# Optimization experiments

Measured on AMD Instinct MI355X. Metric: run time of the kernel, lower is better.

The kernel has to match this reference:

```python
import jax, jax.numpy as jnp
import numpy as np

DIM = 512
NUM_HEADS = 8
HEAD_DIM = DIM // NUM_HEADS


def setup_inputs() -> dict:
    key = jax.random.key(0)
    ks = jax.random.split(key, 9)
    s = 1.0 / np.sqrt(DIM)
    x = jax.random.normal(ks[0], (2, 4096, DIM), dtype=jnp.float32)
    Wq = jax.random.uniform(ks[1], (DIM, DIM), jnp.float32, -s, s)
    bq = jax.random.uniform(ks[2], (DIM,), jnp.float32, -s, s)
    Wk = jax.random.uniform(ks[3], (DIM, DIM), jnp.float32, -s, s)
    bk = jax.random.uniform(ks[4], (DIM,), jnp.float32, -s, s)
    Wv = jax.random.uniform(ks[5], (DIM, DIM), jnp.float32, -s, s)
    bv = jax.random.uniform(ks[6], (DIM,), jnp.float32, -s, s)
    Wo = jax.random.uniform(ks[7], (DIM, DIM), jnp.float32, -s, s)
    bo = jax.random.uniform(ks[8], (DIM,), jnp.float32, -s, s)
    return {"x": x, "Wq": Wq, "bq": bq, "Wk": Wk, "bk": bk,
            "Wv": Wv, "bv": bv, "Wo": Wo, "bo": bo}


def reference(x, Wq, bq, Wk, bk, Wv, bv, Wo, bo):
    B, S, D = x.shape
    H, Hd = NUM_HEADS, HEAD_DIM
    # Linear layers (torch stores weight as [out,in]; here W is [in,out])
    q = (x @ Wq + bq).reshape(B, S, H, Hd).transpose(0, 2, 1, 3)  # [B,H,S,Hd]
    k = (x @ Wk + bk).reshape(B, S, H, Hd).transpose(0, 2, 1, 3)
    v = (x @ Wv + bv).reshape(B, S, H, Hd).transpose(0, 2, 1, 3)
    # NOTE: original scales by dim**0.5, not head_dim**0.5
    energy = jnp.einsum('bhqd,bhkd->bhqk', q, k) / jnp.sqrt(jnp.float32(D))
    attn = jax.nn.softmax(energy, axis=-1)
    out = jnp.einsum('bhqk,bhkd->bhqd', attn, v)
    out = out.transpose(0, 2, 1, 3).reshape(B, S, D)
    return out @ Wo + bo
```

## Files before the change

kernel.cpp:

```cpp
#include <hip/hip_runtime.h>

typedef unsigned short USH;
typedef short s16x8 __attribute__((ext_vector_type(8)));
typedef float f32x4 __attribute__((ext_vector_type(4)));
typedef float f32x4v __attribute__((ext_vector_type(4)));
typedef unsigned int u32x4 __attribute__((ext_vector_type(4)));
typedef s16x8 s16x8_a __attribute__((may_alias));
typedef f32x4v f32x4v_a __attribute__((may_alias));
typedef u32x4 u32x4_a __attribute__((may_alias));
typedef unsigned long long u64_a __attribute__((may_alias));

#if __has_builtin(__builtin_amdgcn_exp2f)
#define EXP2F(x) __builtin_amdgcn_exp2f(x)
#else
#define EXP2F(x) __builtin_exp2f(x)
#endif

__device__ __forceinline__ USH f2bf(float f) {
  union { float f; unsigned int i; } c; c.f = f;
  unsigned int x = c.i;
  return (USH)((x + 0x7FFFu + ((x >> 16) & 1u)) >> 16);
}
__device__ __forceinline__ unsigned int pk_bf16(float a, float b) {
#if __has_builtin(__builtin_amdgcn_cvt_pk_bf16_f32)
  typedef USH ush2 __attribute__((ext_vector_type(2)));
  union { ush2 v; unsigned int u; } r;
  r.v = __builtin_amdgcn_cvt_pk_bf16_f32(a, b);
  return r.u;
#else
  union { float f; unsigned int i; } ca, cb; ca.f = a; cb.f = b;
  return ((ca.i + 0x8000u) >> 16) | ((cb.i + 0x8000u) & 0xFFFF0000u);
#endif
}

__device__ __forceinline__ f32x4 mfma16(s16x8 a, s16x8 b, f32x4 c) {
  return __builtin_amdgcn_mfma_f32_16x16x32_bf16(a, b, c, 0, 0, 0);
}

#if __has_builtin(__builtin_amdgcn_global_load_lds)
__device__ __forceinline__ void gld_lds16(const void* g, void* l) {
  __builtin_amdgcn_global_load_lds(
      static_cast<const unsigned int __attribute__((address_space(1)))*>(
          (const void __attribute__((address_space(1)))*)g),
      static_cast<unsigned int __attribute__((address_space(3)))*>(
          (void __attribute__((address_space(3)))*)l),
      16, 0, 0);
}
#else
__device__ __forceinline__ void gld_lds16(const void* g, void* l) {
  *(s16x8_a*)l = *(const s16x8_a*)g;
}
#endif

__global__ __launch_bounds__(256) void prep(
    const float* __restrict__ Wq, const float* __restrict__ Wk,
    const float* __restrict__ Wv, const float* __restrict__ Wo,
    USH* __restrict__ wsT) {
  __shared__ float tile[32][33];
  const int z = blockIdx.z;
  const int t = threadIdx.x;
  const float* W = (z == 0) ? Wq : (z == 1) ? Wk : (z == 2) ? Wv : Wo;
  USH* WT = wsT + (size_t)z * 262144;
  const int n0 = blockIdx.x * 32, k0 = blockIdx.y * 32;
  const int tx = t & 31, ty = t >> 5;
  #pragma unroll
  for (int i = 0; i < 4; ++i)
    tile[ty + i * 8][tx] = W[(size_t)(k0 + ty + i * 8) * 512 + n0 + tx];
  __syncthreads();
  #pragma unroll
  for (int i = 0; i < 4; ++i)
    WT[(size_t)(n0 + ty + i * 8) * 512 + k0 + tx] = f2bf(tile[tx][ty + i * 8]);
}

template <int MODE>
__global__ __launch_bounds__(256, 3) void gemm_bias(
    const USH* __restrict__ A, const float* __restrict__ A32,
    const USH* __restrict__ BT0,
    const float* __restrict__ b0, const float* __restrict__ b1,
    const float* __restrict__ b2,
    USH* __restrict__ oQ, USH* __restrict__ oKV, float* __restrict__ oF) {
  __shared__ __align__(16) USH As[MODE == 1 ? 16384 : 8192];
  __shared__ __align__(16) USH Bs[8192];
  const int z = blockIdx.z;
  const USH* BT = BT0 + (size_t)z * 262144;
  const float* bias = (z == 0) ? b0 : ((z == 1) ? b1 : b2);
  USH* outb = (z == 0) ? oQ : (oKV + (size_t)(z - 1) * 4194304);
  const float qs = (MODE == 1 && z == 0) ? 0.06375871528132839f : 1.0f;

  const int t = threadIdx.x;
  const int w = t >> 6, lane = t & 63;
  const int c = lane & 15, g = lane >> 4;
  const int wm = w & 1, wn = w >> 1;
  const int m0 = blockIdx.x * 128, n0 = blockIdx.y * 128;

  f32x4 acc[4][4] = {};

  const int rB = w * 32 + (lane >> 3);
  const int ccB = (((lane & 7) ^ ((lane >> 3) & 7))) * 8;
  const USH* BpD = BT + (size_t)(n0 + rB) * 512 + ccB;
  USH* lB = Bs + w * 2048 + lane * 8;

  const USH* ApD = nullptr;
  USH* lA0 = nullptr;
  const float* Ap32 = nullptr;
  USH* lA1 = nullptr;
  if (MODE == 0) {
    ApD = A + (size_t)(m0 + rB) * 512 + ccB;
    lA0 = As + w * 2048 + lane * 8;
  } else {
    const int rA = w * 4 + (lane >> 4);
    const int gcA = (lane & 15) ^ (rA & 15);
    Ap32 = A32 + (size_t)(m0 + rA) * 512 + gcA * 4;
    lA1 = As + w * 512 + lane * 8;
  }

  for (int kt = 0; kt < 8; ++kt) {
    __syncthreads();
    if (MODE == 0) {
      #pragma unroll
      for (int j = 0; j < 4; ++j) {
        gld_lds16(ApD + kt * 64 + j * 4096, lA0 + j * 512);
        gld_lds16(BpD + kt * 64 + j * 4096, lB + j * 512);
      }
    } else {
      #pragma unroll
      for (int j = 0; j < 8; ++j)
        gld_lds16(Ap32 + kt * 64 + (size_t)j * 8192, lA1 + j * 2048);
      #pragma unroll
      for (int j = 0; j < 4; ++j)
        gld_lds16(BpD + kt * 64 + j * 4096, lB + j * 512);
    }
    __syncthreads();
    #pragma unroll
    for (int ks = 0; ks < 2; ++ks) {
      s16x8 af[4], bfr[4];
      #pragma unroll
      for (int i = 0; i < 4; ++i) {
        const int ra = wm * 64 + i * 16 + c;
        const int rb = wn * 64 + i * 16 + c;
        if (MODE == 0) {
          af[i] = *(const s16x8_a*)(As + ra * 64 + ((ks * 4 + g) ^ (ra & 7)) * 8);
        } else {
          const int e = ks * 4 + g;
          const int p0 = (2 * e) ^ (ra & 15), p1 = (2 * e + 1) ^ (ra & 15);
          const float* Af = (const float*)As + ra * 64;
          const f32x4v lo = *(const f32x4v_a*)(Af + p0 * 4);
          const f32x4v hi = *(const f32x4v_a*)(Af + p1 * 4);
          union { u32x4 u; s16x8 v; } cvt;
          cvt.u.x = pk_bf16(lo.x, lo.y); cvt.u.y = pk_bf16(lo.z, lo.w);
          cvt.u.z = pk_bf16(hi.x, hi.y); cvt.u.w = pk_bf16(hi.z, hi.w);
          af[i] = cvt.v;
        }
        bfr[i] = *(const s16x8_a*)(Bs + rb * 64 + ((ks * 4 + g) ^ (rb & 7)) * 8);
      }
      #pragma unroll
      for (int mf = 0; mf < 4; ++mf)
        #pragma unroll
        for (int nf = 0; nf < 4; ++nf)
          acc[mf][nf] = mfma16(af[mf], bfr[nf], acc[mf][nf]);
    }
  }

  #pragma unroll
  for (int nf = 0; nf < 4; ++nf) {
    const int n = n0 + wn * 64 + nf * 16 + c;
    const float bv = bias[n];
    #pragma unroll
    for (int mf = 0; mf < 4; ++mf)
      #pragma unroll
      for (int r = 0; r < 4; ++r) {
        const int m = m0 + wm * 64 + mf * 16 + g * 4 + r;
        const float v = (acc[mf][nf][r] + bv) * qs;
        if (MODE == 0) {
          oF[(size_t)m * 512 + n] = v;
        } else {
          const int bb = m >> 12, s = m & 4095, h = n >> 6, hd = n & 63;
          if (z == 2)
            outb[(((size_t)(bb * 8 + h)) * 64 + hd) * 4096 + s] = f2bf(v);
          else
            outb[(((size_t)(bb * 8 + h)) * 4096 + s) * 64 + hd] = f2bf(v);
        }
      }
  }
}

__global__ __launch_bounds__(512, 2) void attn(const USH* __restrict__ Qbuf,
                                               const USH* __restrict__ kv,
                                               USH* __restrict__ att) {
  __shared__ __align__(16) USH Ks[2 * 8192];
  __shared__ __align__(16) USH Vt[2 * 8192];
  __shared__ __align__(16) USH Ps[8][32 * 140];
  __shared__ float lbuf[8][32];

  const int t = threadIdx.x;
  const int w = t >> 6, lane = t & 63;
  const int c = lane & 15, g = lane >> 4;
  const int linear = blockIdx.x + (blockIdx.y << 4);
  const int xcd = linear & 7, idx = linear >> 3;
  const int bh = xcd + ((idx >> 4) << 3);
  const int bb = bh >> 3, hh = bh & 7;
  const size_t base = (size_t)bh * 262144;
  const USH* Q = Qbuf + base;
  const USH* K = kv + base;
  const USH* V = kv + 4194304 + base;
  const int q0 = (idx & 15) * 256 + w * 32;

  s16x8 qf[2][2];
  #pragma unroll
  for (int qi = 0; qi < 2; ++qi)
    #pragma unroll
    for (int kh = 0; kh < 2; ++kh)
      qf[qi][kh] = *(const s16x8_a*)(Q + (size_t)(q0 + qi * 16 + c) * 64 + kh * 32 + g * 8);

  s16x8 onesf;
  {
    const short one = (short)0x3F80, val = (c == 0) ? one : (short)0;
    #pragma unroll
    for (int j = 0; j < 8; ++j) onesf[j] = val;
  }

  f32x4 o[2][4] = {};
  f32x4 o_l[2] = {};

  const int keyK = w * 16 + (lane >> 2);
  const int ccK = (lane & 3) ^ ((keyK >> 1) & 3);
  const USH* gK0 = K + (size_t)keyK * 64 + ccK * 8;
  const int hdV = w * 4 + (lane >> 4);
  const int ccV = (lane & 15) ^ (hdV & 7);
  const USH* gV0 = V + (size_t)hdV * 4096 + ccV * 8;
  USH* lK = Ks + w * 512 + lane * 8;
  USH* lV = Vt + w * 512 + lane * 8;

  #pragma unroll
  for (int j = 0; j < 2; ++j) {
    gld_lds16(gK0 + j * 32, lK + j * 4096);
    gld_lds16(gV0 + (size_t)j * 131072, lV + j * 4096);
  }

  for (int kt = 0; kt < 32; ++kt) {
    const int buf = kt & 1;
    __syncthreads();
    if (kt < 31) {
      const int nb = (buf ^ 1) * 8192;
      #pragma unroll
      for (int j = 0; j < 2; ++j) {
        gld_lds16(gK0 + (size_t)(kt + 1) * 8192 + j * 32, lK + nb + j * 4096);
        gld_lds16(gV0 + (size_t)(kt + 1) * 128 + (size_t)j * 131072, lV + nb + j * 4096);
      }
    }

    f32x4 st[2][8] = {};
    #pragma unroll
    for (int kh = 0; kh < 2; ++kh) {
      s16x8 ak[8];
      #pragma unroll
      for (int kff = 0; kff < 8; ++kff) {
        const int row = kff * 16 + c;
        const int qsw = (g ^ ((c >> 1) & 3)) * 8;
        ak[kff] = *(const s16x8_a*)(Ks + buf * 8192 + kh * 4096 + row * 32 + qsw);
      }
      #pragma unroll
      for (int qi = 0; qi < 2; ++qi)
        #pragma unroll
        for (int kff = 0; kff < 8; ++kff)
          st[qi][kff] = mfma16(ak[kff], qf[qi][kh], st[qi][kff]);
    }

    #pragma unroll
    for (int qi = 0; qi < 2; ++qi)
      #pragma unroll
      for (int kff = 0; kff < 8; ++kff) {
        #pragma unroll
        for (int r = 0; r < 4; ++r) st[qi][kff][r] = EXP2F(st[qi][kff][r]);
        const unsigned int lo = pk_bf16(st[qi][kff][0], st[qi][kff][1]);
        const unsigned int hi = pk_bf16(st[qi][kff][2], st[qi][kff][3]);
        *(u64_a*)(&Ps[w][(qi * 16 + c) * 140 + kff * 16 + g * 4]) =
            (unsigned long long)lo | ((unsigned long long)hi << 32);
      }

    #pragma unroll
    for (int kf = 0; kf < 4; ++kf) {
      s16x8 ap[2];
      #pragma unroll
      for (int qi = 0; qi < 2; ++qi)
        ap[qi] = *(const s16x8_a*)(&Ps[w][(qi * 16 + c) * 140 + kf * 32 + g * 8]);
      s16x8 bv[4];
      #pragma unroll
      for (int hf = 0; hf < 4; ++hf) {
        const int qv = (((kf * 4 + g) ^ (c & 7))) * 8;
        bv[hf] = *(const s16x8_a*)(Vt + buf * 8192 + (c + 16 * hf) * 128 + qv);
      }
      #pragma unroll
      for (int qi = 0; qi < 2; ++qi) {
        #pragma unroll
        for (int hf = 0; hf < 4; ++hf)
          o[qi][hf] = mfma16(ap[qi], bv[hf], o[qi][hf]);
        o_l[qi] = mfma16(ap[qi], onesf, o_l[qi]);
      }
    }
  }

  if (c == 0) {
    #pragma unroll
    for (int qi = 0; qi < 2; ++qi)
      #pragma unroll
      for (int r = 0; r < 4; ++r) lbuf[w][qi * 16 + g * 4 + r] = o_l[qi][r];
  }
  __syncthreads();

  #pragma unroll
  for (int qi = 0; qi < 2; ++qi)
    #pragma unroll
    for (int r = 0; r < 4; ++r) {
      const int ml = qi * 16 + g * 4 + r;
      const float linv = 1.0f / lbuf[w][ml];
      const int qrow = q0 + ml;
      #pragma unroll
      for (int hf = 0; hf < 4; ++hf) {
        const int hd = c + 16 * hf;
        att[((size_t)(bb * 4096 + qrow)) * 512 + hh * 64 + hd] =
            f2bf(o[qi][hf][r] * linv);
      }
    }
}

extern "C" void kernel_launch(void* const* d_in, const int* in_sizes, int n_in,
                              void* d_out, int out_size, void* d_ws, size_t ws_size,
                              hipStream_t stream) {
  (void)in_sizes; (void)n_in; (void)out_size; (void)ws_size;
  const float* x  = (const float*)d_in[0];
  const float* Wq = (const float*)d_in[1];
  const float* bq = (const float*)d_in[2];
  const float* Wk = (const float*)d_in[3];
  const float* bk = (const float*)d_in[4];
  const float* Wv = (const float*)d_in[5];
  const float* bv = (const float*)d_in[6];
  const float* Wo = (const float*)d_in[7];
  const float* bo = (const float*)d_in[8];
  USH* ws  = (USH*)d_ws;
  USH* wT  = ws;
  USH* kv  = ws + 1048576;
  USH* att = ws + 1048576 + 8388608;
  float* outF = (float*)d_out;
  USH* qscratch = (USH*)d_out;

  prep<<<dim3(16, 16, 4), 256, 0, stream>>>(Wq, Wk, Wv, Wo, wT);
  gemm_bias<1><<<dim3(64, 4, 3), 256, 0, stream>>>(nullptr, x, wT, bq, bk, bv,
                                                   qscratch, kv, nullptr);
  attn<<<dim3(16, 16), 512, 0, stream>>>(qscratch, kv, att);
  gemm_bias<0><<<dim3(64, 4, 1), 256, 0, stream>>>(att, nullptr, wT + 3 * 262144,
                                                   bo, bo, bo,
                                                   nullptr, nullptr, outF);
}
```

Before: 204.0 us.

## Rewrite attention with 32x32 MFMA, register-resident P, and smaller blocks

Rewrites the attention kernel to use 32x32x16 bf16 MFMAs with K as the A operand. This keeps the exp'd scores in registers, exchanging them across lane halves with a shuffle instead of round-tripping P through LDS. Blocks shrink to 4 waves covering 128 queries, with twice as many blocks and software interleaving of QK and PV across key sub-blocks. The output is staged through LDS so global stores are 16-byte and coalesced. The cost is more register pressure and shuffles, and a different LDS swizzle.

```diff
diff --git a/kernel.cpp b/kernel.cpp
--- a/kernel.cpp
+++ b/kernel.cpp
@@ -3,12 +3,13 @@
 typedef unsigned short USH;
 typedef short s16x8 __attribute__((ext_vector_type(8)));
 typedef float f32x4 __attribute__((ext_vector_type(4)));
+typedef float f32x16 __attribute__((ext_vector_type(16)));
 typedef float f32x4v __attribute__((ext_vector_type(4)));
 typedef unsigned int u32x4 __attribute__((ext_vector_type(4)));
 typedef s16x8 s16x8_a __attribute__((may_alias));
 typedef f32x4v f32x4v_a __attribute__((may_alias));
 typedef u32x4 u32x4_a __attribute__((may_alias));
-typedef unsigned long long u64_a __attribute__((may_alias));
+typedef unsigned int u32_a __attribute__((may_alias));
 
 #if __has_builtin(__builtin_amdgcn_exp2f)
 #define EXP2F(x) __builtin_amdgcn_exp2f(x)
@@ -35,6 +36,9 @@
 
 __device__ __forceinline__ f32x4 mfma16(s16x8 a, s16x8 b, f32x4 c) {
   return __builtin_amdgcn_mfma_f32_16x16x32_bf16(a, b, c, 0, 0, 0);
+}
+__device__ __forceinline__ f32x16 mfma32(s16x8 a, s16x8 b, f32x16 c) {
+  return __builtin_amdgcn_mfma_f32_32x32x16_bf16(a, b, c, 0, 0, 0);
 }
 
 #if __has_builtin(__builtin_amdgcn_global_load_lds)
@@ -184,144 +188,124 @@
   }
 }
 
-__global__ __launch_bounds__(512, 2) void attn(const USH* __restrict__ Qbuf,
+__global__ __launch_bounds__(256, 2) void attn(const USH* __restrict__ Qbuf,
                                                const USH* __restrict__ kv,
                                                USH* __restrict__ att) {
   __shared__ __align__(16) USH Ks[2 * 8192];
   __shared__ __align__(16) USH Vt[2 * 8192];
-  __shared__ __align__(16) USH Ps[8][32 * 140];
-  __shared__ float lbuf[8][32];
 
   const int t = threadIdx.x;
   const int w = t >> 6, lane = t & 63;
-  const int c = lane & 15, g = lane >> 4;
-  const int linear = blockIdx.x + (blockIdx.y << 4);
+  const int cq = lane & 31, hq = lane >> 5;
+  const int linear = blockIdx.x + (blockIdx.y << 5);
   const int xcd = linear & 7, idx = linear >> 3;
-  const int bh = xcd + ((idx >> 4) << 3);
+  const int bh = xcd + ((idx >> 5) << 3);
   const int bb = bh >> 3, hh = bh & 7;
   const size_t base = (size_t)bh * 262144;
   const USH* Q = Qbuf + base;
   const USH* K = kv + base;
   const USH* V = kv + 4194304 + base;
-  const int q0 = (idx & 15) * 256 + w * 32;
-
-  s16x8 qf[2][2];
-  #pragma unroll
-  for (int qi = 0; qi < 2; ++qi)
-    #pragma unroll
-    for (int kh = 0; kh < 2; ++kh)
-      qf[qi][kh] = *(const s16x8_a*)(Q + (size_t)(q0 + qi * 16 + c) * 64 + kh * 32 + g * 8);
-
-  s16x8 onesf;
-  {
-    const short one = (short)0x3F80, val = (c == 0) ? one : (short)0;
-    #pragma unroll
-    for (int j = 0; j < 8; ++j) onesf[j] = val;
-  }
-
-  f32x4 o[2][4] = {};
-  f32x4 o_l[2] = {};
-
-  const int keyK = w * 16 + (lane >> 2);
-  const int ccK = (lane & 3) ^ ((keyK >> 1) & 3);
-  const USH* gK0 = K + (size_t)keyK * 64 + ccK * 8;
-  const int hdV = w * 4 + (lane >> 4);
-  const int ccV = (lane & 15) ^ (hdV & 7);
-  const USH* gV0 = V + (size_t)hdV * 4096 + ccV * 8;
-  USH* lK = Ks + w * 512 + lane * 8;
-  USH* lV = Vt + w * 512 + lane * 8;
-
-  #pragma unroll
-  for (int j = 0; j < 2; ++j) {
-    gld_lds16(gK0 + j * 32, lK + j * 4096);
-    gld_lds16(gV0 + (size_t)j * 131072, lV + j * 4096);
-  }
+  const int q0 = (idx & 31) * 128 + w * 32;
+
+  s16x8 qB[4];
+  #pragma unroll
+  for (int t4 = 0; t4 < 4; ++t4)
+    qB[t4] = *(const s16x8_a*)(Q + (size_t)(q0 + cq) * 64 + t4 * 16 + hq * 8);
+
+  s16x8 ones;
+  #pragma unroll
+  for (int j = 0; j < 8; ++j) ones[j] = (short)0x3F80;
+
+  f32x16 o[2] = {};
+  f32x16 ol = {};
+
+  const int rK = t >> 3;
+  const USH* gK0 = K + (size_t)rK * 64 + (((t & 7) ^ (rK & 7)) * 8);
+  const int rV = t >> 4;
+  const USH* gV0 = V + (size_t)rV * 4096 + (((t & 15) ^ (rV & 7)) * 8);
+  USH* lK = Ks + t * 8;
+  USH* lV = Vt + t * 8;
+
+  auto DMA = [&](int kt, int buf) {
+    #pragma unroll
+    for (int j = 0; j < 4; ++j) {
+      gld_lds16(gK0 + (size_t)kt * 8192 + j * 2048, lK + buf + j * 2048);
+      gld_lds16(gV0 + (size_t)kt * 128 + (size_t)j * 65536, lV + buf + j * 2048);
+    }
+  };
+
+  auto QK = [&](int kb, int buf) -> f32x16 {
+    f32x16 st = {};
+    #pragma unroll
+    for (int t4 = 0; t4 < 4; ++t4) {
+      const s16x8 ka = *(const s16x8_a*)(
+          Ks + buf + (kb * 32 + cq) * 64 + (((2 * t4 + hq) ^ (cq & 7)) * 8));
+      st = mfma32(ka, qB[t4], st);
+    }
+    return st;
+  };
+
+  auto SMPV = [&](f32x16 st, int kb, int buf) {
+    unsigned int P[8], X[8];
+    #pragma unroll
+    for (int i = 0; i < 8; ++i)
+      P[i] = pk_bf16(EXP2F(st[2 * i]), EXP2F(st[2 * i + 1]));
+    #pragma unroll
+    for (int i = 0; i < 8; ++i)
+      X[i] = __shfl_xor(P[i], 32);
+    #pragma unroll
+    for (int ks = 0; ks < 2; ++ks) {
+      union { u32x4 u; s16x8 v; } bf;
+      bf.u.x = hq ? X[4 * ks + 2] : P[4 * ks];
+      bf.u.y = hq ? X[4 * ks + 3] : P[4 * ks + 1];
+      bf.u.z = hq ? P[4 * ks + 2] : X[4 * ks];
+      bf.u.w = hq ? P[4 * ks + 3] : X[4 * ks + 1];
+      const s16x8 bks = bf.v;
+      #pragma unroll
+      for (int hb = 0; hb < 2; ++hb) {
+        const s16x8 va = *(const s16x8_a*)(
+            Vt + buf + (hb * 32 + cq) * 128 +
+            (((4 * kb + 2 * ks + hq) ^ (cq & 7)) * 8));
+        o[hb] = mfma32(va, bks, o[hb]);
+      }
+      ol = mfma32(ones, bks, ol);
+    }
+  };
+
+  DMA(0, 0);
 
   for (int kt = 0; kt < 32; ++kt) {
-    const int buf = kt & 1;
+    const int buf = (kt & 1) * 8192;
     __syncthreads();
-    if (kt < 31) {
-      const int nb = (buf ^ 1) * 8192;
-      #pragma unroll
-      for (int j = 0; j < 2; ++j) {
-        gld_lds16(gK0 + (size_t)(kt + 1) * 8192 + j * 32, lK + nb + j * 4096);
-        gld_lds16(gV0 + (size_t)(kt + 1) * 128 + (size_t)j * 131072, lV + nb + j * 4096);
-      }
-    }
-
-    f32x4 st[2][8] = {};
-    #pragma unroll
-    for (int kh = 0; kh < 2; ++kh) {
-      s16x8 ak[8];
-      #pragma unroll
-      for (int kff = 0; kff < 8; ++kff) {
-        const int row = kff * 16 + c;
-        const int qsw = (g ^ ((c >> 1) & 3)) * 8;
-        ak[kff] = *(const s16x8_a*)(Ks + buf * 8192 + kh * 4096 + row * 32 + qsw);
-      }
-      #pragma unroll
-      for (int qi = 0; qi < 2; ++qi)
-        #pragma unroll
-        for (int kff = 0; kff < 8; ++kff)
-          st[qi][kff] = mfma16(ak[kff], qf[qi][kh], st[qi][kff]);
-    }
-
-    #pragma unroll
-    for (int qi = 0; qi < 2; ++qi)
-      #pragma unroll
-      for (int kff = 0; kff < 8; ++kff) {
-        #pragma unroll
-        for (int r = 0; r < 4; ++r) st[qi][kff][r] = EXP2F(st[qi][kff][r]);
-        const unsigned int lo = pk_bf16(st[qi][kff][0], st[qi][kff][1]);
-        const unsigned int hi = pk_bf16(st[qi][kff][2], st[qi][kff][3]);
-        *(u64_a*)(&Ps[w][(qi * 16 + c) * 140 + kff * 16 + g * 4]) =
-            (unsigned long long)lo | ((unsigned long long)hi << 32);
-      }
-
-    #pragma unroll
-    for (int kf = 0; kf < 4; ++kf) {
-      s16x8 ap[2];
-      #pragma unroll
-      for (int qi = 0; qi < 2; ++qi)
-        ap[qi] = *(const s16x8_a*)(&Ps[w][(qi * 16 + c) * 140 + kf * 32 + g * 8]);
-      s16x8 bv[4];
-      #pragma unroll
-      for (int hf = 0; hf < 4; ++hf) {
-        const int qv = (((kf * 4 + g) ^ (c & 7))) * 8;
-        bv[hf] = *(const s16x8_a*)(Vt + buf * 8192 + (c + 16 * hf) * 128 + qv);
-      }
-      #pragma unroll
-      for (int qi = 0; qi < 2; ++qi) {
-        #pragma unroll
-        for (int hf = 0; hf < 4; ++hf)
-          o[qi][hf] = mfma16(ap[qi], bv[hf], o[qi][hf]);
-        o_l[qi] = mfma16(ap[qi], onesf, o_l[qi]);
-      }
-    }
-  }
-
-  if (c == 0) {
-    #pragma unroll
-    for (int qi = 0; qi < 2; ++qi)
-      #pragma unroll
-      for (int r = 0; r < 4; ++r) lbuf[w][qi * 16 + g * 4 + r] = o_l[qi][r];
-  }
+    if (kt < 31) DMA(kt + 1, buf ^ 8192);
+    f32x16 stA = QK(0, buf);
+    f32x16 stB = QK(1, buf);
+    SMPV(stA, 0, buf);
+    stA = QK(2, buf);
+    SMPV(stB, 1, buf);
+    stB = QK(3, buf);
+    SMPV(stA, 2, buf);
+    SMPV(stB, 3, buf);
+  }
+
   __syncthreads();
-
-  #pragma unroll
-  for (int qi = 0; qi < 2; ++qi)
-    #pragma unroll
-    for (int r = 0; r < 4; ++r) {
-      const int ml = qi * 16 + g * 4 + r;
-      const float linv = 1.0f / lbuf[w][ml];
-      const int qrow = q0 + ml;
-      #pragma unroll
-      for (int hf = 0; hf < 4; ++hf) {
-        const int hd = c + 16 * hf;
-        att[((size_t)(bb * 4096 + qrow)) * 512 + hh * 64 + hd] =
-            f2bf(o[qi][hf][r] * linv);
-      }
-    }
+  USH* scr = Ks + w * 2304;
+  const float linv = 1.0f / ol[0];
+  #pragma unroll
+  for (int hb = 0; hb < 2; ++hb)
+    #pragma unroll
+    for (int i = 0; i < 8; ++i) {
+      const int hd = hb * 32 + 4 * hq + 2 * (i & 1) + 8 * (i >> 1);
+      const unsigned int pw =
+          pk_bf16(o[hb][2 * i] * linv, o[hb][2 * i + 1] * linv);
+      *(u32_a*)(scr + cq * 72 + hd) = pw;
+    }
+  #pragma unroll
+  for (int p = 0; p < 4; ++p) {
+    const int row = p * 8 + (lane >> 3), col = (lane & 7) * 8;
+    const s16x8 v = *(const s16x8_a*)(scr + row * 72 + col);
+    *(s16x8_a*)(att + ((size_t)(bb * 4096 + q0 + row)) * 512 + hh * 64 + col) = v;
+  }
 }
 
 extern "C" void kernel_launch(void* const* d_in, const int* in_sizes, int n_in,
@@ -347,7 +331,7 @@
   prep<<<dim3(16, 16, 4), 256, 0, stream>>>(Wq, Wk, Wv, Wo, wT);
   gemm_bias<1><<<dim3(64, 4, 3), 256, 0, stream>>>(nullptr, x, wT, bq, bk, bv,
                                                    qscratch, kv, nullptr);
-  attn<<<dim3(16, 16), 512, 0, stream>>>(qscratch, kv, att);
+  attn<<<dim3(32, 16), 256, 0, stream>>>(qscratch, kv, att);
   gemm_bias<0><<<dim3(64, 4, 1), 256, 0, stream>>>(att, nullptr, wT + 3 * 262144,
                                                    bo, bo, bo,
                                                    nullptr, nullptr, outF);
```

New measurement: 212.2 us. 4.0% more time.
